# Kernel optimization log

Measured on AMD Instinct MI355X. Metric: run time of the kernel, lower is better.

Reference implementation:

```python
import jax, jax.numpy as jnp
import numpy as np

HIDDEN_DIM = 2048
NUM_HEADS = 16
HEAD_DIM = HIDDEN_DIM // NUM_HEADS
BATCH = 2
SEQ = 2048


def setup_inputs() -> dict:
    key = jax.random.key(0)
    ks = jax.random.split(key, 5)
    scale = 1.0 / np.sqrt(HIDDEN_DIM)
    x = jax.random.normal(ks[0], (BATCH, SEQ, HIDDEN_DIM), dtype=jnp.float32)
    w_q = jax.random.normal(ks[1], (HIDDEN_DIM, HIDDEN_DIM), dtype=jnp.float32) * scale
    w_k = jax.random.normal(ks[2], (HIDDEN_DIM, HIDDEN_DIM), dtype=jnp.float32) * scale
    w_v = jax.random.normal(ks[3], (HIDDEN_DIM, HIDDEN_DIM), dtype=jnp.float32) * scale
    w_o = jax.random.normal(ks[4], (HIDDEN_DIM, HIDDEN_DIM), dtype=jnp.float32) * scale
    return {"x": x, "w_q": w_q, "w_k": w_k, "w_v": w_v, "w_o": w_o}


def reference(x, w_q, w_k, w_v, w_o):
    # Projections: x @ W.T  (weights stored as (out, in) like torch)
    q = jnp.einsum('bsd,ed->bse', x, w_q)
    k = jnp.einsum('bsd,ed->bse', x, w_k)
    v = jnp.einsum('bsd,ed->bse', x, w_v)
    b, s, _ = q.shape
    # split heads: (b, h, s, hd)
    q = q.reshape(b, s, NUM_HEADS, HEAD_DIM).transpose(0, 2, 1, 3)
    k = k.reshape(b, s, NUM_HEADS, HEAD_DIM).transpose(0, 2, 1, 3)
    v = v.reshape(b, s, NUM_HEADS, HEAD_DIM).transpose(0, 2, 1, 3)
    scale = 1.0 / np.sqrt(HEAD_DIM)
    # Online-softmax tiling in the source (causal=False default) is
    # mathematically identical to standard softmax attention.
    scores = jnp.einsum('bhqd,bhkd->bhqk', q, k) * scale
    p = jax.nn.softmax(scores, axis=-1)
    o = jnp.einsum('bhqk,bhkd->bhqd', p, v)
    o = o.transpose(0, 2, 1, 3).reshape(b, s, HIDDEN_DIM)
    return jnp.einsum('bsd,ed->bse', o, w_o)
```

## Files before the change

### kernel.cpp

```cpp
#include <hip/hip_runtime.h>


typedef _Float16 half8 __attribute__((ext_vector_type(8)));
typedef _Float16 half4 __attribute__((ext_vector_type(4)));
typedef float floatx4 __attribute__((ext_vector_type(4)));

__device__ __forceinline__ void async16(const void* g, void* l) {
  __builtin_amdgcn_global_load_lds((__attribute__((address_space(1))) void*)(g),
                                   (__attribute__((address_space(3))) void*)(l),
                                   16, 0, 0);
}

__global__ void cvt_all(const float* __restrict__ x, const float* __restrict__ w0,
                        const float* __restrict__ w1, const float* __restrict__ w2,
                        const float* __restrict__ w3, _Float16* __restrict__ xh,
                        _Float16* __restrict__ wh, float scale0) {
  int i = blockIdx.x * blockDim.x + threadIdx.x;
  const int XQ = 1 << 21;
  float sc = 1.0f;
  const float* src;
  _Float16* dst;
  int j;
  if (i < XQ) { src = x; dst = xh; j = i; }
  else {
    int t = i - XQ;
    int m = t >> 20;
    src = (m == 0) ? w0 : (m == 1) ? w1 : (m == 2) ? w2 : w3;
    if (m == 0) sc = scale0;
    dst = wh; j = t;
  }
  int js = (i < XQ) ? j : (j & ((1 << 20) - 1));
  float4 v = reinterpret_cast<const float4*>(src)[js];
  union { _Float16 h[4]; short4 s; } u;
  u.h[0] = (_Float16)(v.x * sc); u.h[1] = (_Float16)(v.y * sc);
  u.h[2] = (_Float16)(v.z * sc); u.h[3] = (_Float16)(v.w * sc);
  reinterpret_cast<short4*>(dst)[j] = u.s;
}

__device__ __forceinline__ void rdA4(half8 (&f)[4][2], const _Float16* base,
                                     int ch0, int ch1) {
#pragma unroll
  for (int mt = 0; mt < 4; ++mt) {
    f[mt][0] = *reinterpret_cast<const half8*>(base + mt * 2048 + ch0);
    f[mt][1] = *reinterpret_cast<const half8*>(base + mt * 2048 + ch1);
  }
}
__device__ __forceinline__ void rdB2(half8 (&f)[2][2], const _Float16* base,
                                     int ch0, int ch1) {
#pragma unroll
  for (int nt = 0; nt < 2; ++nt) {
    f[nt][0] = *reinterpret_cast<const half8*>(base + nt * 4096 + ch0);
    f[nt][1] = *reinterpret_cast<const half8*>(base + nt * 4096 + ch1);
  }
}
template <int MO, int NO>
__device__ __forceinline__ void mmg16(floatx4 (&acc)[8][4], const half8 (&af)[4][2],
                                      const half8 (&bf)[2][2]) {
#pragma unroll
  for (int kk = 0; kk < 2; ++kk)
#pragma unroll
    for (int mt = 0; mt < 4; ++mt)
#pragma unroll
      for (int nt = 0; nt < 2; ++nt)
        acc[MO + mt][NO + nt] = __builtin_amdgcn_mfma_f32_16x16x32_f16(
            af[mt][kk], bf[nt][kk], acc[MO + mt][NO + nt], 0, 0, 0);
}

#define STAGE_AH0(buf, kk) { async16(ags + (kk), &(buf)[ldst]); \
                             async16(ags + 131072 + (kk), &(buf)[4096 + ldst]); }
#define STAGE_AH1(buf, kk) { async16(ags + 262144 + (kk), &(buf)[8192 + ldst]); \
                             async16(ags + 393216 + (kk), &(buf)[12288 + ldst]); }
#define STAGE_BH0(buf, kk) { async16(bgs + (kk), &(buf)[ldst]); \
                             async16(bgs + 131072 + (kk), &(buf)[4096 + ldst]); }
#define STAGE_BH1(buf, kk) { async16(bgs + 262144 + (kk), &(buf)[8192 + ldst]); \
                             async16(bgs + 393216 + (kk), &(buf)[12288 + ldst]); }
#define VMW(n) asm volatile("s_waitcnt vmcnt(" #n ")" ::: "memory")
#define SBAR() __builtin_amdgcn_s_barrier()
#define SCHED() __builtin_amdgcn_sched_barrier(0)
#define PRIO1() __builtin_amdgcn_s_setprio(1)
#define PRIO0() __builtin_amdgcn_s_setprio(0)

__global__ __launch_bounds__(512, 2)
void gemm_nt(const _Float16* __restrict__ A, const _Float16* __restrict__ Bw,
             void* __restrict__ Cv, void* __restrict__ Cv2) {
  __shared__ _Float16 As[2][256 * 64];
  __shared__ _Float16 Bs[2][256 * 64];
  const int tid = threadIdx.x;
  const int wave = tid >> 6, lane = tid & 63;
  const int wm = wave >> 2, wn = wave & 3;
  const int l15 = lane & 15, l4 = lane >> 4;

  const int NBN = 24;
  const int nwg = NBN * 16;
  const int swz = (blockIdx.x & 7) * (nwg >> 3) + (blockIdx.x >> 3);
  const int bn = swz % NBN, bm = swz / NBN;

  const int srow = tid >> 3;
  const int g = (tid & 7) ^ (srow & 7);
  const _Float16* ags = A + (size_t)(bm * 256 + srow) * 2048 + g * 8;
  const _Float16* bgs = Bw + (size_t)(bn * 256 + srow) * 2048 + g * 8;
  const int ldst = tid * 8;

  const int arow = wm * 16 + l15;
  const int brow = wn * 16 + l15;
  const int ch0 = (l4 ^ (l15 & 7)) * 8;
  const int ch1 = ((l4 + 4) ^ (l15 & 7)) * 8;

  STAGE_AH0(As[0], 0); STAGE_BH0(Bs[0], 0);
  STAGE_BH1(Bs[0], 0); STAGE_AH1(As[0], 0);
  STAGE_AH0(As[1], 64); STAGE_BH0(Bs[1], 64);
  VMW(4);
  SBAR();

  floatx4 acc[8][4] = {};
  half8 afA[4][2], afB[4][2], bfA[2][2], bfB[2][2];
  rdA4(afA, &As[0][arow * 64], ch0, ch1);
  rdB2(bfA, &Bs[0][brow * 64], ch0, ch1);

#pragma unroll 2
  for (int t = 0; t < 30; ++t) {
    const int c = t & 1, nx = c ^ 1;
    const int k1 = t * 64 + 64, k2 = t * 64 + 128;
    const _Float16* Ac = &As[c][0];
    const _Float16* Bc = &Bs[c][0];

    PRIO1(); mmg16<0, 0>(acc, afA, bfA); PRIO0();
    rdB2(bfB, Bc + brow * 64 + 8192, ch0, ch1);
    STAGE_BH1(Bs[nx], k1);
    SCHED(); VMW(6); SBAR();

    PRIO1(); mmg16<0, 2>(acc, afA, bfB); PRIO0();
    rdA4(afB, Ac + arow * 64 + 8192, ch0, ch1);
    STAGE_AH1(As[nx], k1);
    SCHED(); VMW(6); SBAR();

    PRIO1(); mmg16<4, 0>(acc, afB, bfA); PRIO0();
    STAGE_AH0(As[c], k2);
    SCHED(); VMW(6); SBAR();

    PRIO1(); mmg16<4, 2>(acc, afB, bfB); PRIO0();
    rdA4(afA, &As[nx][arow * 64], ch0, ch1);
    rdB2(bfA, &Bs[nx][brow * 64], ch0, ch1);
    STAGE_BH0(Bs[c], k2);
    SCHED(); VMW(6); SBAR();
  }

  {
    const _Float16* Ac = &As[0][0];
    const _Float16* Bc = &Bs[0][0];
    PRIO1(); mmg16<0, 0>(acc, afA, bfA); PRIO0();
    rdB2(bfB, Bc + brow * 64 + 8192, ch0, ch1);
    STAGE_BH1(Bs[1], 1984);
    SCHED(); VMW(6); SBAR();

    PRIO1(); mmg16<0, 2>(acc, afA, bfB); PRIO0();
    rdA4(afB, Ac + arow * 64 + 8192, ch0, ch1);
    STAGE_AH1(As[1], 1984);
    SCHED(); VMW(6); SBAR();

    PRIO1(); mmg16<4, 0>(acc, afB, bfA); PRIO0();
    SCHED(); VMW(4); SBAR();

    PRIO1(); mmg16<4, 2>(acc, afB, bfB); PRIO0();
    rdA4(afA, &As[1][arow * 64], ch0, ch1);
    rdB2(bfA, &Bs[1][brow * 64], ch0, ch1);
    SCHED(); VMW(2); SBAR();
  }
  {
    const _Float16* Ac = &As[1][0];
    const _Float16* Bc = &Bs[1][0];
    PRIO1(); mmg16<0, 0>(acc, afA, bfA); PRIO0();
    rdB2(bfB, Bc + brow * 64 + 8192, ch0, ch1);
    SCHED(); VMW(0); SBAR();
    PRIO1(); mmg16<0, 2>(acc, afA, bfB); PRIO0();
    rdA4(afB, Ac + arow * 64 + 8192, ch0, ch1);
    mmg16<4, 0>(acc, afB, bfA);
    mmg16<4, 2>(acc, afB, bfB);
  }

  const int cb0 = bn * 256;
  if (cb0 < 4096) {
    _Float16* C = (_Float16*)Cv + (size_t)(cb0 >> 11) * (4096ull * 2048);
#pragma unroll
    for (int mt = 0; mt < 8; ++mt)
#pragma unroll
      for (int nt = 0; nt < 4; ++nt) {
        int r0 = bm * 256 + mt * 32 + wm * 16 + l4 * 4;
        int cg = (cb0 + nt * 64 + wn * 16 + l15) & 2047;
#pragma unroll
        for (int r = 0; r < 4; ++r)
          C[(size_t)(r0 + r) * 2048 + cg] = (_Float16)acc[mt][nt][r];
      }
  } else {
    _Float16* C = (_Float16*)Cv2;
#pragma unroll
    for (int mt = 0; mt < 8; ++mt)
#pragma unroll
      for (int nt = 0; nt < 4; ++nt) {
        int m0 = bm * 256 + mt * 32 + wm * 16 + l4 * 4;
        int d = cb0 + nt * 64 + wn * 16 + l15 - 4096;
        size_t base = (size_t)(m0 >> 11) * (2048ull * 2048) + (size_t)d * 2048 + (m0 & 2047);
        union { _Float16 h[4]; short4 s; } u;
#pragma unroll
        for (int r = 0; r < 4; ++r) u.h[r] = (_Float16)acc[mt][nt][r];
        *reinterpret_cast<short4*>(C + base) = u.s;
      }
  }
}

__global__ __launch_bounds__(256)
void gemm_wo(const _Float16* __restrict__ A, const _Float16* __restrict__ Bw,
             float* __restrict__ C) {
  __shared__ _Float16 As[128 * 64];
  __shared__ _Float16 Bs[128 * 64];
  const int tid = threadIdx.x;
  const int wave = tid >> 6, lane = tid & 63;
  const int wm = wave >> 1, wn = wave & 1;
  const int l15 = lane & 15, l4 = lane >> 4;
  const int bm = blockIdx.y, bn = blockIdx.x;

  floatx4 acc[4][4] = {};

  for (int k0 = 0; k0 < 2048; k0 += 64) {
    __syncthreads();
#pragma unroll
    for (int i = 0; i < 4; ++i) {
      int c = i * 256 + tid;
      int row = c >> 3, cc = c & 7;
      int gg = cc ^ (row & 7);
      async16(A + (size_t)(bm * 128 + row) * 2048 + k0 + gg * 8, &As[c * 8]);
      async16(Bw + (size_t)(bn * 128 + row) * 2048 + k0 + gg * 8, &Bs[c * 8]);
    }
    __syncthreads();
#pragma unroll
    for (int ks = 0; ks < 2; ++ks) {
      half8 af[4], bf[4];
      int ch = (ks * 4 + l4) ^ (l15 & 7);
#pragma unroll
      for (int t = 0; t < 4; ++t) {
        af[t] = *reinterpret_cast<const half8*>(&As[(wm * 64 + t * 16 + l15) * 64 + ch * 8]);
        bf[t] = *reinterpret_cast<const half8*>(&Bs[(wn * 64 + t * 16 + l15) * 64 + ch * 8]);
      }
#pragma unroll
      for (int mt = 0; mt < 4; ++mt)
#pragma unroll
        for (int nt = 0; nt < 4; ++nt)
          acc[mt][nt] = __builtin_amdgcn_mfma_f32_16x16x32_f16(af[mt], bf[nt], acc[mt][nt], 0, 0, 0);
    }
  }

  const int rbase = bm * 128 + wm * 64;
  const int cbase = bn * 128 + wn * 64;
#pragma unroll
  for (int mt = 0; mt < 4; ++mt)
#pragma unroll
    for (int nt = 0; nt < 4; ++nt) {
      int r0 = rbase + mt * 16 + l4 * 4;
      int cg = cbase + nt * 16 + l15;
#pragma unroll
      for (int r = 0; r < 4; ++r)
        C[(size_t)(r0 + r) * 2048 + cg] = acc[mt][nt][r];
    }
}

__global__ __launch_bounds__(256, 2)
void flash_attn(const _Float16* __restrict__ Q, const _Float16* __restrict__ Kg,
                const _Float16* __restrict__ Vt, _Float16* __restrict__ O) {
  __shared__ _Float16 Ks[64 * 128];
  __shared__ _Float16 Vs[128 * 64];
  __shared__ _Float16 Ps[128 * 64];
  const int tid = threadIdx.x, wave = tid >> 6, lane = tid & 63;
  const int l15 = lane & 15, l4 = lane >> 4;
  const int bh = blockIdx.y, b = bh >> 4, h = bh & 15;
  const int q0 = blockIdx.x * 128;

  const _Float16* Qp = Q + ((size_t)(b * 2048 + q0 + wave * 32)) * 2048 + h * 128;
  const _Float16* Kp = Kg + (size_t)b * 2048 * 2048 + h * 128;
  const _Float16* Vp = Vt + (size_t)b * 2048 * 2048 + (size_t)(h * 128) * 2048;

  half8 qf[2][4];
#pragma unroll
  for (int qt = 0; qt < 2; ++qt)
#pragma unroll
    for (int ks = 0; ks < 4; ++ks)
      qf[qt][ks] = *reinterpret_cast<const half8*>(
          Qp + (size_t)(qt * 16 + l15) * 2048 + ks * 32 + l4 * 8);

  floatx4 oacc[2][8] = {};
  float lsumq[2] = {0.f, 0.f};

  for (int k0 = 0; k0 < 2048; k0 += 64) {
    __syncthreads();
#pragma unroll
    for (int i = 0; i < 4; ++i) {
      int c = i * 256 + tid;
      int row = c >> 4, cc = c & 15;
      int g = cc ^ (row & 15);
      async16(Kp + (size_t)(k0 + row) * 2048 + g * 8, &Ks[c * 8]);
    }
#pragma unroll
    for (int i = 0; i < 4; ++i) {
      int c = i * 256 + tid;
      int row = c >> 3, cc = c & 7;
      int g = cc ^ (row & 7);
      async16(Vp + (size_t)row * 2048 + k0 + g * 8, &Vs[c * 8]);
    }
    __syncthreads();

    floatx4 sacc[4][2] = {};
#pragma unroll
    for (int ks = 0; ks < 4; ++ks) {
      half8 kf[4];
#pragma unroll
      for (int st = 0; st < 4; ++st) {
        int row = st * 16 + l15;
        int ch = (ks * 4 + l4) ^ l15;
        kf[st] = *reinterpret_cast<const half8*>(&Ks[row * 128 + ch * 8]);
      }
#pragma unroll
      for (int st = 0; st < 4; ++st)
#pragma unroll
        for (int qt = 0; qt < 2; ++qt)
          sacc[st][qt] = __builtin_amdgcn_mfma_f32_16x16x32_f16(kf[st], qf[qt][ks], sacc[st][qt], 0, 0, 0);
    }

#pragma unroll
    for (int qt = 0; qt < 2; ++qt)
#pragma unroll
      for (int st = 0; st < 4; ++st) {
        float p0 = exp2f(sacc[st][qt][0]);
        float p1 = exp2f(sacc[st][qt][1]);
        float p2 = exp2f(sacc[st][qt][2]);
        float p3 = exp2f(sacc[st][qt][3]);
        lsumq[qt] += (p0 + p1) + (p2 + p3);
        half4 pv;
        pv[0] = (_Float16)p0; pv[1] = (_Float16)p1;
        pv[2] = (_Float16)p2; pv[3] = (_Float16)p3;
        int ch = (st * 2 + (l4 >> 1)) ^ (l15 & 7);
        *reinterpret_cast<half4*>(
            &Ps[(wave * 32 + qt * 16 + l15) * 64 + ch * 8 + (l4 & 1) * 4]) = pv;
      }

    __builtin_amdgcn_s_waitcnt(0xC07F);

#pragma unroll
    for (int ks2 = 0; ks2 < 2; ++ks2) {
      half8 pf[2];
#pragma unroll
      for (int mt = 0; mt < 2; ++mt)
        pf[mt] = *reinterpret_cast<const half8*>(
            &Ps[(wave * 32 + mt * 16 + l15) * 64 + (((ks2 * 4 + l4) ^ (l15 & 7)) * 8)]);
#pragma unroll
      for (int nt2 = 0; nt2 < 8; ++nt2) {
        int row = nt2 * 16 + l15;
        int ch = (ks2 * 4 + l4) ^ (row & 7);
        half8 vf = *reinterpret_cast<const half8*>(&Vs[row * 64 + ch * 8]);
#pragma unroll
        for (int mt = 0; mt < 2; ++mt)
          oacc[mt][nt2] = __builtin_amdgcn_mfma_f32_16x16x32_f16(pf[mt], vf, oacc[mt][nt2], 0, 0, 0);
      }
    }
  }

#pragma unroll
  for (int qt = 0; qt < 2; ++qt) {
    lsumq[qt] += __shfl_xor(lsumq[qt], 16);
    lsumq[qt] += __shfl_xor(lsumq[qt], 32);
  }

  _Float16* Op = O + ((size_t)(b * 2048 + q0 + wave * 32)) * 2048 + h * 128;
#pragma unroll
  for (int mt = 0; mt < 2; ++mt)
#pragma unroll
    for (int r = 0; r < 4; ++r) {
      float inv = 1.0f / __shfl(lsumq[mt], l4 * 4 + r);
#pragma unroll
      for (int nt2 = 0; nt2 < 8; ++nt2) {
        int row = mt * 16 + l4 * 4 + r;
        int col = nt2 * 16 + l15;
        Op[(size_t)row * 2048 + col] = (_Float16)(oacc[mt][nt2][r] * inv);
      }
    }
}

extern "C" void kernel_launch(void* const* d_in, const int* in_sizes, int n_in,
                              void* d_out, int out_size, void* d_ws, size_t ws_size,
                              hipStream_t stream) {
  const float* x = (const float*)d_in[0];
  const float* wq = (const float*)d_in[1];
  const float* wk = (const float*)d_in[2];
  const float* wv = (const float*)d_in[3];
  const float* wo = (const float*)d_in[4];
  float* out = (float*)d_out;

  const size_t XN = (size_t)4096 * 2048;
  const size_t WN = (size_t)2048 * 2048;
  _Float16* xh = (_Float16*)d_ws;
  _Float16* qh = xh + XN;
  _Float16* vth = xh + 3 * XN;
  _Float16* oh = xh + 4 * XN;
  _Float16* wqh = xh + 5 * XN;

  const float SM_SCALE = 0.08838834764831845f * 1.4426950408889634f;

  cvt_all<<<dim3(24576), 256, 0, stream>>>(x, wq, wk, wv, wo, xh, wqh, SM_SCALE);
  gemm_nt<<<dim3(384), 512, 0, stream>>>(xh, wqh, qh, vth);
  flash_attn<<<dim3(16, 32), 256, 0, stream>>>(qh, qh + XN, vth, oh);
  gemm_wo<<<dim3(16, 32), 256, 0, stream>>>(oh, wqh + 3 * WN, out);
}
```

Measured before the change: 396.0 us.

## Prefetch next K/V tile into registers during flash attention compute

```diff
diff --git a/kernel.cpp b/kernel.cpp
--- a/kernel.cpp
+++ b/kernel.cpp
@@ -278,6 +278,25 @@
   const _Float16* Kp = Kg + (size_t)b * 2048 * 2048 + h * 128;
   const _Float16* Vp = Vt + (size_t)b * 2048 * 2048 + (size_t)(h * 128) * 2048;
 
+  const _Float16* ka[4]; const _Float16* va[4];
+  int kl[4], vl[4];
+#pragma unroll
+  for (int i = 0; i < 4; ++i) {
+    int c = i * 256 + tid;
+    int row = c >> 4, cc = c & 15, gk = cc ^ (row & 15);
+    ka[i] = Kp + (size_t)row * 2048 + gk * 8;
+    kl[i] = c * 8;
+    int rv = c >> 3, cv = c & 7, gv = cv ^ (rv & 7);
+    va[i] = Vp + (size_t)rv * 2048 + gv * 8;
+    vl[i] = c * 8;
+  }
+
+  int4 kreg[4], vreg[4];
+#pragma unroll
+  for (int i = 0; i < 4; ++i) kreg[i] = *reinterpret_cast<const int4*>(ka[i]);
+#pragma unroll
+  for (int i = 0; i < 4; ++i) vreg[i] = *reinterpret_cast<const int4*>(va[i]);
+
   half8 qf[2][4];
 #pragma unroll
   for (int qt = 0; qt < 2; ++qt)
@@ -289,21 +308,20 @@
   floatx4 oacc[2][8] = {};
   float lsumq[2] = {0.f, 0.f};
 
-  for (int k0 = 0; k0 < 2048; k0 += 64) {
+  for (int t = 0; t < 32; ++t) {
     __syncthreads();
 #pragma unroll
-    for (int i = 0; i < 4; ++i) {
-      int c = i * 256 + tid;
-      int row = c >> 4, cc = c & 15;
-      int g = cc ^ (row & 15);
-      async16(Kp + (size_t)(k0 + row) * 2048 + g * 8, &Ks[c * 8]);
-    }
-#pragma unroll
-    for (int i = 0; i < 4; ++i) {
-      int c = i * 256 + tid;
-      int row = c >> 3, cc = c & 7;
-      int g = cc ^ (row & 7);
-      async16(Vp + (size_t)row * 2048 + k0 + g * 8, &Vs[c * 8]);
+    for (int i = 0; i < 4; ++i) *reinterpret_cast<int4*>(&Ks[kl[i]]) = kreg[i];
+#pragma unroll
+    for (int i = 0; i < 4; ++i) *reinterpret_cast<int4*>(&Vs[vl[i]]) = vreg[i];
+    if (t < 31) {
+      const int kn = t * 64 + 64;
+#pragma unroll
+      for (int i = 0; i < 4; ++i)
+        kreg[i] = *reinterpret_cast<const int4*>(ka[i] + (size_t)kn * 2048);
+#pragma unroll
+      for (int i = 0; i < 4; ++i)
+        vreg[i] = *reinterpret_cast<const int4*>(va[i] + kn);
     }
     __syncthreads();
 
```

After: 494.7 us. 1.25x slower.
